# Optimization experiments

Measured on AMD Instinct MI355X. Metric: run time of the kernel, lower is better.

## Reference

```python
import jax, jax.numpy as jnp
import numpy as np

HIDDEN = 1024
N_HEADS = 16
HEAD_DIM = HIDDEN // N_HEADS


def _rope_tables(seq_len, dim, dtype):
    inv_freq = 1.0 / (10000.0 ** (jnp.arange(0, dim, 2, dtype=jnp.float32) / dim))
    t = jnp.arange(seq_len, dtype=jnp.float32)
    freqs = jnp.einsum('i,j->ij', t, inv_freq)          # [S, dim/2]
    emb = jnp.concatenate([freqs, freqs], axis=-1)       # [S, dim]
    cos = jnp.cos(emb)[None, :, None, :].astype(dtype)   # [1, S, 1, dim]
    sin = jnp.sin(emb)[None, :, None, :].astype(dtype)
    return cos, sin


def _rotate_half(x):
    x1, x2 = x[..., : x.shape[-1] // 2], x[..., x.shape[-1] // 2 :]
    return jnp.concatenate([-x2, x1], axis=-1)


def setup_inputs() -> dict:
    key = jax.random.key(0)
    ks = jax.random.split(key, 9)
    s = 1.0 / np.sqrt(HIDDEN)
    return {
        'x': jax.random.normal(ks[0], (2, 2048, HIDDEN), dtype=jnp.float32),
        'q_w': jax.random.uniform(ks[1], (HIDDEN, HIDDEN), jnp.float32, -s, s),
        'q_b': jax.random.uniform(ks[2], (HIDDEN,), jnp.float32, -s, s),
        'k_w': jax.random.uniform(ks[3], (HIDDEN, HIDDEN), jnp.float32, -s, s),
        'k_b': jax.random.uniform(ks[4], (HIDDEN,), jnp.float32, -s, s),
        'v_w': jax.random.uniform(ks[5], (HIDDEN, HIDDEN), jnp.float32, -s, s),
        'v_b': jax.random.uniform(ks[6], (HIDDEN,), jnp.float32, -s, s),
        'o_w': jax.random.uniform(ks[7], (HIDDEN, HIDDEN), jnp.float32, -s, s),
        'o_b': jax.random.uniform(ks[8], (HIDDEN,), jnp.float32, -s, s),
    }


def reference(x, q_w, q_b, k_w, k_b, v_w, v_b, o_w, o_b):
    B, S, _ = x.shape
    scale = HEAD_DIM ** -0.5
    # projections (torch Linear: x @ W.T + b)
    q = (x @ q_w.T + q_b).reshape(B, S, N_HEADS, HEAD_DIM)
    k = (x @ k_w.T + k_b).reshape(B, S, N_HEADS, HEAD_DIM)
    v = (x @ v_w.T + v_b).reshape(B, S, N_HEADS, HEAD_DIM)
    # RoPE
    cos, sin = _rope_tables(S, HEAD_DIM, x.dtype)
    q = q * cos + _rotate_half(q) * sin
    k = k * cos + _rotate_half(k) * sin
    # attention: [B, H, S, S]
    scores = jnp.einsum('bqhd,bkhd->bhqk', q, k) * scale
    attn = jax.nn.softmax(scores, axis=-1)
    out = jnp.einsum('bhqk,bkhd->bqhd', attn, v).reshape(B, S, HIDDEN)
    return out @ o_w.T + o_b
```

## Files before the change

kernel.cpp:

```cpp
#include <hip/hip_runtime.h>
#include <hip/hip_bf16.h>


#define SEQ    2048
#define BATCH  2
#define NHEADS 16
#define HDIM   64
#define HID    1024
#define NTOK   (BATCH*SEQ)

typedef __bf16 bf16x8 __attribute__((ext_vector_type(8)));
typedef float  f32x4  __attribute__((ext_vector_type(4)));
typedef unsigned short u16x8 __attribute__((ext_vector_type(8)));

__device__ __forceinline__ unsigned short bfc(float x) {
  return __builtin_bit_cast(unsigned short, (__bf16)x);
}
#define EXP2(x) __builtin_amdgcn_exp2f(x)

__device__ __forceinline__ void gload16(const void* gptr, void* ldsptr) {
  typedef __attribute__((address_space(3))) unsigned int as3_uint;
  typedef const __attribute__((address_space(1))) unsigned int as1_uint;
  __builtin_amdgcn_global_load_lds(
      (as1_uint*)(unsigned long long)gptr,
      (as3_uint*)(unsigned int)(unsigned long long)ldsptr,
      16, 0, 0);
}

__device__ __forceinline__ void cvt8(const float* __restrict__ s,
                                     unsigned short* __restrict__ d, int i) {
  float4 a = *reinterpret_cast<const float4*>(s + i);
  float4 b = *reinterpret_cast<const float4*>(s + i + 4);
  u16x8 o;
  o[0] = bfc(a.x); o[1] = bfc(a.y); o[2] = bfc(a.z); o[3] = bfc(a.w);
  o[4] = bfc(b.x); o[5] = bfc(b.y); o[6] = bfc(b.z); o[7] = bfc(b.w);
  *reinterpret_cast<u16x8*>(d + i) = o;
}

__global__ __launch_bounds__(256) void prep(
    const float* __restrict__ x,
    const float* __restrict__ qw, const float* __restrict__ kw,
    const float* __restrict__ vw, const float* __restrict__ ow,
    unsigned short* __restrict__ xb,
    unsigned short* __restrict__ wqb, unsigned short* __restrict__ wkb,
    unsigned short* __restrict__ wvb, unsigned short* __restrict__ wob,
    float* __restrict__ ct, float* __restrict__ st)
{
  const int XN = NTOK * HID / 8;
  const int WN = HID * HID / 8;
  int tid = blockIdx.x * 256 + threadIdx.x;
  if (tid < XN) {
    cvt8(x, xb, tid * 8);
  } else if (tid < XN + 4 * WN) {
    int r = tid - XN;
    int which = r >> 17;
    int i = (r & (WN - 1)) * 8;
    const float* s = (which == 0) ? qw : (which == 1) ? kw : (which == 2) ? vw : ow;
    unsigned short* d = (which == 0) ? wqb : (which == 1) ? wkb : (which == 2) ? wvb : wob;
    cvt8(s, d, i);
  } else {
    int idx = tid - (XN + 4 * WN);
    if (idx < SEQ * 32) {
      int p = idx >> 5, j = idx & 31;
      float inv = powf(10000.0f, -(float)(2 * j) * (1.0f / 64.0f));
      float a = (float)p * inv;
      ct[idx] = cosf(a);
      st[idx] = sinf(a);
    }
  }
}

__global__ __launch_bounds__(256) void gemm_qkv(
    const unsigned short* __restrict__ X,
    const unsigned short* __restrict__ Wq, const unsigned short* __restrict__ Wk,
    const unsigned short* __restrict__ Wv,
    const float* __restrict__ bq, const float* __restrict__ bk, const float* __restrict__ bv,
    const float* __restrict__ ct, const float* __restrict__ st,
    unsigned short* __restrict__ Qo, unsigned short* __restrict__ Ko,
    unsigned short* __restrict__ VTo)
{
  __shared__ unsigned short LSH[16384];
  const int z = blockIdx.z;
  const unsigned short* W = (z == 0) ? Wq : (z == 1) ? Wk : Wv;
  const float* bias = (z == 0) ? bq : (z == 1) ? bk : bv;
  const int tm = blockIdx.x, tn = blockIdx.y;
  const int t = threadIdx.x, w = t >> 6, l = t & 63;
  const int wm = w >> 1, wn = w & 1, g = l >> 4;

  f32x4 acc[4][4] = {};

  const int arow0 = tm * 128, brow0 = tn * 128;
  const int s0 = w * 2, s1 = w * 2 + 1;
  const int r0 = s0 * 16 + (l >> 2), r1 = s1 * 16 + (l >> 2);
  const int kc = (l & 3) * 8;

#define GSTAGE(buf, k0)                                                            \
  {                                                                                \
    gload16(X + (long)(arow0 + r0) * HID + (k0) + kc, LSH + (buf) * 4096 + s0 * 512); \
    gload16(X + (long)(arow0 + r1) * HID + (k0) + kc, LSH + (buf) * 4096 + s1 * 512); \
    gload16(W + (long)(brow0 + r0) * HID + (k0) + kc, LSH + 8192 + (buf) * 4096 + s0 * 512); \
    gload16(W + (long)(brow0 + r1) * HID + (k0) + kc, LSH + 8192 + (buf) * 4096 + s1 * 512); \
  }

  GSTAGE(0, 0)
  asm volatile("s_waitcnt vmcnt(0)" ::: "memory");
  __builtin_amdgcn_s_barrier();
  int cur = 0;
  for (int k0 = 0; k0 < HID; k0 += 32) {
    if (k0 + 32 < HID) GSTAGE(cur ^ 1, k0 + 32)
    bf16x8 af[4], bfr[4];
#pragma unroll
    for (int fm = 0; fm < 4; ++fm)
      af[fm] = *reinterpret_cast<const bf16x8*>(
          LSH + cur * 4096 + (wm * 64 + fm * 16 + (l & 15)) * 32 + g * 8);
#pragma unroll
    for (int fn = 0; fn < 4; ++fn)
      bfr[fn] = *reinterpret_cast<const bf16x8*>(
          LSH + 8192 + cur * 4096 + (wn * 64 + fn * 16 + (l & 15)) * 32 + g * 8);
    __builtin_amdgcn_s_setprio(1);
#pragma unroll
    for (int fm = 0; fm < 4; ++fm)
#pragma unroll
      for (int fn = 0; fn < 4; ++fn)
        acc[fm][fn] = __builtin_amdgcn_mfma_f32_16x16x32_bf16(af[fm], bfr[fn], acc[fm][fn], 0, 0, 0);
    __builtin_amdgcn_s_setprio(0);
    asm volatile("s_waitcnt vmcnt(0)" ::: "memory");
    __builtin_amdgcn_s_barrier();
    cur ^= 1;
  }
#undef GSTAGE

  const int colb = brow0 + wn * 64;
  float bsv[4];
#pragma unroll
  for (int fn = 0; fn < 4; ++fn) bsv[fn] = bias[colb + fn * 16 + (l & 15)];

  if (z == 2) {
#pragma unroll
    for (int fm = 0; fm < 4; ++fm) {
      int tok = wm * 64 + fm * 16 + g * 4;
#pragma unroll
      for (int fn = 0; fn < 4; ++fn) {
        int col = wn * 64 + fn * 16 + (l & 15);
        unsigned int u0 = (unsigned int)bfc(acc[fm][fn][0] + bsv[fn]) |
                          ((unsigned int)bfc(acc[fm][fn][1] + bsv[fn]) << 16);
        unsigned int u1 = (unsigned int)bfc(acc[fm][fn][2] + bsv[fn]) |
                          ((unsigned int)bfc(acc[fm][fn][3] + bsv[fn]) << 16);
        uint2 uv; uv.x = u0; uv.y = u1;
        *reinterpret_cast<uint2*>(&LSH[col * 128 + (tok ^ ((col & 7) << 3))]) = uv;
      }
    }
    __syncthreads();
    const int bb = arow0 >> 11, stok = arow0 & (SEQ - 1);
#pragma unroll
    for (int p8 = 0; p8 < 8; ++p8) {
      int col = p8 * 16 + (t >> 4);
      int soff = (t & 15) * 8;
      uint4 v = *reinterpret_cast<const uint4*>(&LSH[col * 128 + (soff ^ ((col & 7) << 3))]);
      int hh = (brow0 + col) >> 6;
      int dd = col & 63;
      unsigned short* dst = VTo + ((long)(bb * NHEADS + hh) * HDIM + dd) * SEQ + stok + soff;
      *reinterpret_cast<uint4*>(dst) = v;
    }
    return;
  }

  unsigned short* Out = (z == 0) ? Qo : Ko;
  const int h = colb >> 6;
#pragma unroll
  for (int fm = 0; fm < 4; ++fm) {
#pragma unroll
    for (int r = 0; r < 4; ++r) {
      int grow = arow0 + wm * 64 + fm * 16 + g * 4 + r;
      int b = grow >> 11, sidx = grow & (SEQ - 1);
      unsigned short* ob = Out + ((long)(b * NHEADS + h) * SEQ + sidx) * HDIM;
#pragma unroll
      for (int fn2 = 0; fn2 < 2; ++fn2) {
        int d1 = fn2 * 16 + (l & 15);
        float v1 = acc[fm][fn2][r] + bsv[fn2];
        float v2 = acc[fm][fn2 + 2][r] + bsv[fn2 + 2];
        float c = ct[sidx * 32 + d1], sn = st[sidx * 32 + d1];
        float o1 = v1 * c - v2 * sn;
        float o2 = v2 * c + v1 * sn;
        if (z == 0) { o1 *= 0.18033688f; o2 *= 0.18033688f; }
        ob[d1] = bfc(o1);
        ob[d1 + 32] = bfc(o2);
      }
    }
  }
}

__global__ __launch_bounds__(256) void attn(
    const unsigned short* __restrict__ Qb,
    const unsigned short* __restrict__ Kb,
    const unsigned short* __restrict__ VTb,
    unsigned short* __restrict__ Ob)
{
  __shared__ unsigned short Kl[2][64 * 64];
  __shared__ unsigned short Vl[2][64 * 64];
  __shared__ unsigned short Pl[4][32 * 64];
  const int bh = blockIdx.x, qt = blockIdx.y;
  const int b = bh >> 4, h = bh & 15;
  const int t = threadIdx.x, w = t >> 6, l = t & 63;
  const long hb = (long)bh * SEQ * HDIM;
  const int g = l >> 4;
  const int swz = (l & 7) << 4;

  const int q0 = qt * 128 + w * 32;
  bf16x8 qf[2][2];
#pragma unroll
  for (int f = 0; f < 2; ++f)
#pragma unroll
    for (int ks = 0; ks < 2; ++ks)
      qf[f][ks] = *reinterpret_cast<const bf16x8*>(
          Qb + hb + (long)(q0 + f * 16 + (l & 15)) * HDIM + ks * 32 + g * 8);

  f32x4 oacc[2][4] = {};
  float lrun[2] = {0.f, 0.f};

  const int srow = l >> 3;
  const int scol = (((l & 7) * 16) ^ ((l >> 3) << 4)) >> 1;
#define STAGE(buf, kt)                                                          \
  {                                                                             \
    gload16(Kb + hb + (long)((kt) + w * 16 + srow) * HDIM + scol,               \
            (char*)Kl[buf] + w * 2048);                                         \
    gload16(Kb + hb + (long)((kt) + w * 16 + 8 + srow) * HDIM + scol,           \
            (char*)Kl[buf] + w * 2048 + 1024);                                  \
    gload16(VTb + hb + (long)(w * 16 + srow) * SEQ + (kt) + scol,               \
            (char*)Vl[buf] + w * 2048);                                         \
    gload16(VTb + hb + (long)(w * 16 + 8 + srow) * SEQ + (kt) + scol,           \
            (char*)Vl[buf] + w * 2048 + 1024);                                  \
  }

  STAGE(0, 0)
  asm volatile("s_waitcnt vmcnt(0)" ::: "memory");
  __builtin_amdgcn_s_barrier();
  int cur = 0;

  for (int it = 0; it < SEQ / 64; ++it) {
    if (it + 1 < SEQ / 64) STAGE(cur ^ 1, (it + 1) * 64)

    f32x4 sa[2][4];
#pragma unroll
    for (int f = 0; f < 2; ++f)
#pragma unroll
      for (int fn = 0; fn < 4; ++fn) sa[f][fn] = f32x4{0.f, 0.f, 0.f, 0.f};
    __builtin_amdgcn_s_setprio(1);
#pragma unroll
    for (int fnK = 0; fnK < 4; ++fnK) {
#pragma unroll
      for (int ks = 0; ks < 2; ++ks) {
        bf16x8 kf = *reinterpret_cast<const bf16x8*>(
            (char*)Kl[cur] + (fnK * 16 + (l & 15)) * 128 + ((ks * 64 + g * 16) ^ swz));
        sa[0][fnK] = __builtin_amdgcn_mfma_f32_16x16x32_bf16(kf, qf[0][ks], sa[0][fnK], 0, 0, 0);
        sa[1][fnK] = __builtin_amdgcn_mfma_f32_16x16x32_bf16(kf, qf[1][ks], sa[1][fnK], 0, 0, 0);
      }
    }
    __builtin_amdgcn_s_setprio(0);

#pragma unroll
    for (int f = 0; f < 2; ++f) {
      float rs = 0.f;
#pragma unroll
      for (int fn = 0; fn < 4; ++fn)
#pragma unroll
        for (int r = 0; r < 4; ++r) {
          float p = EXP2(sa[f][fn][r]);
          sa[f][fn][r] = p;
          rs += p;
        }
      lrun[f] += rs;
    }

#pragma unroll
    for (int f = 0; f < 2; ++f) {
      char* pw = (char*)Pl[w] + (f * 16 + (l & 15)) * 128;
#pragma unroll
      for (int fn = 0; fn < 4; ++fn) {
        unsigned int u0 = (unsigned int)bfc(sa[f][fn][0]) | ((unsigned int)bfc(sa[f][fn][1]) << 16);
        unsigned int u1 = (unsigned int)bfc(sa[f][fn][2]) | ((unsigned int)bfc(sa[f][fn][3]) << 16);
        uint2 uv; uv.x = u0; uv.y = u1;
        *reinterpret_cast<uint2*>(pw + ((fn * 32 + g * 8) ^ swz)) = uv;
      }
    }

    bf16x8 pf[2][2];
#pragma unroll
    for (int f = 0; f < 2; ++f)
#pragma unroll
      for (int ks = 0; ks < 2; ++ks)
        pf[f][ks] = *reinterpret_cast<const bf16x8*>(
            (char*)Pl[w] + (f * 16 + (l & 15)) * 128 + ((ks * 64 + g * 16) ^ swz));
    __builtin_amdgcn_s_setprio(1);
#pragma unroll
    for (int fnD = 0; fnD < 4; ++fnD) {
#pragma unroll
      for (int ks = 0; ks < 2; ++ks) {
        bf16x8 vf = *reinterpret_cast<const bf16x8*>(
            (char*)Vl[cur] + (fnD * 16 + (l & 15)) * 128 + ((ks * 64 + g * 16) ^ swz));
        oacc[0][fnD] = __builtin_amdgcn_mfma_f32_16x16x32_bf16(vf, pf[0][ks], oacc[0][fnD], 0, 0, 0);
        oacc[1][fnD] = __builtin_amdgcn_mfma_f32_16x16x32_bf16(vf, pf[1][ks], oacc[1][fnD], 0, 0, 0);
      }
    }
    __builtin_amdgcn_s_setprio(0);

    asm volatile("s_waitcnt vmcnt(0)" ::: "memory");
    __builtin_amdgcn_s_barrier();
    cur ^= 1;
  }
#undef STAGE

#pragma unroll
  for (int f = 0; f < 2; ++f) {
    float lr = lrun[f];
    lr += __shfl_xor(lr, 16);
    lr += __shfl_xor(lr, 32);
    float inv = 1.0f / lr;
    int q = q0 + f * 16 + (l & 15);
    unsigned short* op = Ob + (long)(b * SEQ + q) * HID + h * HDIM;
#pragma unroll
    for (int fnD = 0; fnD < 4; ++fnD) {
      unsigned int lo = (unsigned int)bfc(oacc[f][fnD][0] * inv) |
                        ((unsigned int)bfc(oacc[f][fnD][1] * inv) << 16);
      unsigned int hi = (unsigned int)bfc(oacc[f][fnD][2] * inv) |
                        ((unsigned int)bfc(oacc[f][fnD][3] * inv) << 16);
      uint2 uv; uv.x = lo; uv.y = hi;
      *reinterpret_cast<uint2*>(op + fnD * 16 + g * 4) = uv;
    }
  }
}

__global__ __launch_bounds__(256) void gemm_o(
    const unsigned short* __restrict__ A,
    const unsigned short* __restrict__ W,
    const float* __restrict__ bias,
    float* __restrict__ Out)
{
  __shared__ unsigned short Al[2][128 * 32];
  __shared__ unsigned short Bl[2][128 * 32];
  const int tm = blockIdx.x, tn = blockIdx.y;
  const int t = threadIdx.x, w = t >> 6, l = t & 63;
  const int wm = w >> 1, wn = w & 1;

  f32x4 acc[4][4] = {};
  const int arow0 = tm * 128, brow0 = tn * 128;
  const int s0 = w * 2, s1 = w * 2 + 1;
  const int r0 = s0 * 16 + (l >> 2), r1 = s1 * 16 + (l >> 2);
  const int kc = (l & 3) * 8;

#define GSTAGE(buf, k0)                                                       \
  {                                                                           \
    gload16(A + (long)(arow0 + r0) * HID + (k0) + kc, Al[buf] + s0 * 512);    \
    gload16(A + (long)(arow0 + r1) * HID + (k0) + kc, Al[buf] + s1 * 512);    \
    gload16(W + (long)(brow0 + r0) * HID + (k0) + kc, Bl[buf] + s0 * 512);    \
    gload16(W + (long)(brow0 + r1) * HID + (k0) + kc, Bl[buf] + s1 * 512);    \
  }

  GSTAGE(0, 0)
  asm volatile("s_waitcnt vmcnt(0)" ::: "memory");
  __builtin_amdgcn_s_barrier();
  int cur = 0;
  for (int k0 = 0; k0 < HID; k0 += 32) {
    if (k0 + 32 < HID) GSTAGE(cur ^ 1, k0 + 32)
    bf16x8 af[4], bfr[4];
#pragma unroll
    for (int fm = 0; fm < 4; ++fm)
      af[fm] = *reinterpret_cast<const bf16x8*>(Al[cur] + (wm * 64 + fm * 16 + (l & 15)) * 32 + (l >> 4) * 8);
#pragma unroll
    for (int fn = 0; fn < 4; ++fn)
      bfr[fn] = *reinterpret_cast<const bf16x8*>(Bl[cur] + (wn * 64 + fn * 16 + (l & 15)) * 32 + (l >> 4) * 8);
    __builtin_amdgcn_s_setprio(1);
#pragma unroll
    for (int fm = 0; fm < 4; ++fm)
#pragma unroll
      for (int fn = 0; fn < 4; ++fn)
        acc[fm][fn] = __builtin_amdgcn_mfma_f32_16x16x32_bf16(af[fm], bfr[fn], acc[fm][fn], 0, 0, 0);
    __builtin_amdgcn_s_setprio(0);
    asm volatile("s_waitcnt vmcnt(0)" ::: "memory");
    __builtin_amdgcn_s_barrier();
    cur ^= 1;
  }
#undef GSTAGE

  const int colb = brow0 + wn * 64;
  float bsv[4];
#pragma unroll
  for (int fn = 0; fn < 4; ++fn) bsv[fn] = bias[colb + fn * 16 + (l & 15)];
#pragma unroll
  for (int fm = 0; fm < 4; ++fm)
#pragma unroll
    for (int r = 0; r < 4; ++r) {
      int grow = arow0 + wm * 64 + fm * 16 + (l >> 4) * 4 + r;
#pragma unroll
      for (int fn = 0; fn < 4; ++fn)
        Out[(long)grow * HID + colb + fn * 16 + (l & 15)] = acc[fm][fn][r] + bsv[fn];
    }
}

extern "C" void kernel_launch(void* const* d_in, const int* in_sizes, int n_in,
                              void* d_out, int out_size, void* d_ws, size_t ws_size,
                              hipStream_t stream) {
  const float* x  = (const float*)d_in[0];
  const float* qw = (const float*)d_in[1];
  const float* qb = (const float*)d_in[2];
  const float* kw = (const float*)d_in[3];
  const float* kb = (const float*)d_in[4];
  const float* vw = (const float*)d_in[5];
  const float* vb = (const float*)d_in[6];
  const float* ow = (const float*)d_in[7];
  const float* ob = (const float*)d_in[8];
  float* out = (float*)d_out;

  char* p = (char*)d_ws;
  unsigned short* xb  = (unsigned short*)p; p += (size_t)NTOK * HID * 2;
  unsigned short* wqb = (unsigned short*)p; p += (size_t)HID * HID * 2;
  unsigned short* wkb = (unsigned short*)p; p += (size_t)HID * HID * 2;
  unsigned short* wvb = (unsigned short*)p; p += (size_t)HID * HID * 2;
  unsigned short* wob = (unsigned short*)p; p += (size_t)HID * HID * 2;
  unsigned short* Qb  = (unsigned short*)p; p += (size_t)NTOK * HID * 2;
  unsigned short* Kb  = (unsigned short*)p; p += (size_t)NTOK * HID * 2;
  unsigned short* VTb = (unsigned short*)p; p += (size_t)NTOK * HID * 2;
  float* ct = (float*)p; p += (size_t)SEQ * 32 * 4;
  float* st = (float*)p; p += (size_t)SEQ * 32 * 4;
  unsigned short* Ab  = xb;

  const int XN = NTOK * HID / 8, WN = HID * HID / 8;
  const int prep_threads = XN + 4 * WN + SEQ * 32;
  prep<<<dim3((prep_threads + 255) / 256), 256, 0, stream>>>(
      x, qw, kw, vw, ow, xb, wqb, wkb, wvb, wob, ct, st);

  gemm_qkv<<<dim3(NTOK / 128, HID / 128, 3), 256, 0, stream>>>(
      xb, wqb, wkb, wvb, qb, kb, vb, ct, st, Qb, Kb, VTb);

  attn<<<dim3(BATCH * NHEADS, SEQ / 128), 256, 0, stream>>>(Qb, Kb, VTb, Ab);

  gemm_o<<<dim3(NTOK / 128, HID / 128), 256, 0, stream>>>(Ab, wob, ob, out);
}
```

Measured before the change: 124.8 us.

## Software-pipeline attention QK and PV across iterations; shrink output GEMM N tile

The attention loop is restructured so that the QK^T MFMAs for tile i run in the same phase as the PV MFMAs for tile i-1. V gets a triple buffer so the staged V tile stays live for one extra iteration, and pointer increments replace recomputed addresses. This is meant to hide the softmax/P round-trip latency behind independent matrix work. Separately, the output GEMM N tile drops from 128 to 64, doubling the block count for better CU occupancy at the cost of more A-tile reloads.

```diff
diff --git a/kernel.cpp b/kernel.cpp
--- a/kernel.cpp
+++ b/kernel.cpp
@@ -197,7 +197,7 @@
     unsigned short* __restrict__ Ob)
 {
   __shared__ unsigned short Kl[2][64 * 64];
-  __shared__ unsigned short Vl[2][64 * 64];
+  __shared__ unsigned short Vl[3][64 * 64];
   __shared__ unsigned short Pl[4][32 * 64];
   const int bh = blockIdx.x, qt = blockIdx.y;
   const int b = bh >> 4, h = bh & 15;
@@ -218,97 +218,126 @@
   f32x4 oacc[2][4] = {};
   float lrun[2] = {0.f, 0.f};
 
+  const int rowq = (l & 15) * 128;
+  const int colx0 = (g * 16) ^ swz;
+  const int colx1 = (64 + g * 16) ^ swz;
+  char* const Pw = (char*)Pl + w * 4096;
+
   const int srow = l >> 3;
   const int scol = (((l & 7) * 16) ^ ((l >> 3) << 4)) >> 1;
-#define STAGE(buf, kt)                                                          \
-  {                                                                             \
-    gload16(Kb + hb + (long)((kt) + w * 16 + srow) * HDIM + scol,               \
-            (char*)Kl[buf] + w * 2048);                                         \
-    gload16(Kb + hb + (long)((kt) + w * 16 + 8 + srow) * HDIM + scol,           \
-            (char*)Kl[buf] + w * 2048 + 1024);                                  \
-    gload16(VTb + hb + (long)(w * 16 + srow) * SEQ + (kt) + scol,               \
-            (char*)Vl[buf] + w * 2048);                                         \
-    gload16(VTb + hb + (long)(w * 16 + 8 + srow) * SEQ + (kt) + scol,           \
-            (char*)Vl[buf] + w * 2048 + 1024);                                  \
-  }
+  const unsigned short* kp0 = Kb + hb + (long)(w * 16 + srow) * HDIM + scol;
+  const unsigned short* kp1 = kp0 + 8 * HDIM;
+  const unsigned short* vp0 = VTb + hb + (long)(w * 16 + srow) * SEQ + scol;
+  const unsigned short* vp1 = vp0 + 8 * SEQ;
+
+#define STAGE(kbuf, vbuf)                                              \
+  {                                                                    \
+    gload16(kp0, (char*)Kl + (kbuf) * 8192 + w * 2048);                \
+    gload16(kp1, (char*)Kl + (kbuf) * 8192 + w * 2048 + 1024);         \
+    gload16(vp0, (char*)Vl + (vbuf) * 8192 + w * 2048);                \
+    gload16(vp1, (char*)Vl + (vbuf) * 8192 + w * 2048 + 1024);         \
+    kp0 += 64 * HDIM; kp1 += 64 * HDIM; vp0 += 64; vp1 += 64;          \
+  }
+
+#define QK(kbuf)                                                                  \
+  _Pragma("unroll")                                                               \
+  for (int f = 0; f < 2; ++f)                                                     \
+    _Pragma("unroll")                                                             \
+    for (int fn = 0; fn < 4; ++fn) sa[f][fn] = f32x4{0.f, 0.f, 0.f, 0.f};         \
+  _Pragma("unroll")                                                               \
+  for (int fnK = 0; fnK < 4; ++fnK) {                                             \
+    const char* kb_ = (char*)Kl + (kbuf) * 8192 + fnK * 2048 + rowq;              \
+    bf16x8 kf0 = *reinterpret_cast<const bf16x8*>(kb_ + colx0);                   \
+    bf16x8 kf1 = *reinterpret_cast<const bf16x8*>(kb_ + colx1);                   \
+    sa[0][fnK] = __builtin_amdgcn_mfma_f32_16x16x32_bf16(kf0, qf[0][0], sa[0][fnK], 0, 0, 0); \
+    sa[0][fnK] = __builtin_amdgcn_mfma_f32_16x16x32_bf16(kf1, qf[0][1], sa[0][fnK], 0, 0, 0); \
+    sa[1][fnK] = __builtin_amdgcn_mfma_f32_16x16x32_bf16(kf0, qf[1][0], sa[1][fnK], 0, 0, 0); \
+    sa[1][fnK] = __builtin_amdgcn_mfma_f32_16x16x32_bf16(kf1, qf[1][1], sa[1][fnK], 0, 0, 0); \
+  }
+
+#define PFREAD                                                                    \
+  _Pragma("unroll")                                                               \
+  for (int f = 0; f < 2; ++f) {                                                   \
+    pf[f][0] = *reinterpret_cast<const bf16x8*>(Pw + f * 2048 + rowq + colx0);    \
+    pf[f][1] = *reinterpret_cast<const bf16x8*>(Pw + f * 2048 + rowq + colx1);    \
+  }
+
+#define PVSTEP(vbuf)                                                              \
+  _Pragma("unroll")                                                               \
+  for (int fnD = 0; fnD < 4; ++fnD) {                                             \
+    const char* vb_ = (char*)Vl + (vbuf) * 8192 + fnD * 2048 + rowq;              \
+    bf16x8 vf0 = *reinterpret_cast<const bf16x8*>(vb_ + colx0);                   \
+    bf16x8 vf1 = *reinterpret_cast<const bf16x8*>(vb_ + colx1);                   \
+    oacc[0][fnD] = __builtin_amdgcn_mfma_f32_16x16x32_bf16(vf0, pf[0][0], oacc[0][fnD], 0, 0, 0); \
+    oacc[0][fnD] = __builtin_amdgcn_mfma_f32_16x16x32_bf16(vf1, pf[0][1], oacc[0][fnD], 0, 0, 0); \
+    oacc[1][fnD] = __builtin_amdgcn_mfma_f32_16x16x32_bf16(vf0, pf[1][0], oacc[1][fnD], 0, 0, 0); \
+    oacc[1][fnD] = __builtin_amdgcn_mfma_f32_16x16x32_bf16(vf1, pf[1][1], oacc[1][fnD], 0, 0, 0); \
+  }
+
+#define SOFTPACK                                                                  \
+  _Pragma("unroll")                                                               \
+  for (int f = 0; f < 2; ++f) {                                                   \
+    float rs = 0.f;                                                               \
+    _Pragma("unroll")                                                             \
+    for (int fn = 0; fn < 4; ++fn)                                                \
+      _Pragma("unroll")                                                           \
+      for (int r = 0; r < 4; ++r) {                                               \
+        float p = EXP2(sa[f][fn][r]);                                             \
+        sa[f][fn][r] = p;                                                         \
+        rs += p;                                                                  \
+      }                                                                           \
+    lrun[f] += rs;                                                                \
+    char* pw_ = Pw + f * 2048 + rowq;                                             \
+    _Pragma("unroll")                                                             \
+    for (int fn = 0; fn < 4; ++fn) {                                              \
+      unsigned int u0 = (unsigned int)bfc(sa[f][fn][0]) | ((unsigned int)bfc(sa[f][fn][1]) << 16); \
+      unsigned int u1 = (unsigned int)bfc(sa[f][fn][2]) | ((unsigned int)bfc(sa[f][fn][3]) << 16); \
+      uint2 uv; uv.x = u0; uv.y = u1;                                             \
+      *reinterpret_cast<uint2*>(pw_ + ((fn * 32 + g * 8) ^ swz)) = uv;            \
+    }                                                                             \
+  }
+
+  f32x4 sa[2][4];
+  bf16x8 pf[2][2];
 
   STAGE(0, 0)
   asm volatile("s_waitcnt vmcnt(0)" ::: "memory");
   __builtin_amdgcn_s_barrier();
-  int cur = 0;
-
-  for (int it = 0; it < SEQ / 64; ++it) {
-    if (it + 1 < SEQ / 64) STAGE(cur ^ 1, (it + 1) * 64)
-
-    f32x4 sa[2][4];
-#pragma unroll
-    for (int f = 0; f < 2; ++f)
-#pragma unroll
-      for (int fn = 0; fn < 4; ++fn) sa[f][fn] = f32x4{0.f, 0.f, 0.f, 0.f};
+
+  STAGE(1, 1)
+  __builtin_amdgcn_s_setprio(1);
+  QK(0)
+  __builtin_amdgcn_s_setprio(0);
+  SOFTPACK
+  asm volatile("s_waitcnt vmcnt(0)" ::: "memory");
+  __builtin_amdgcn_s_barrier();
+
+  int kcur = 1, vr = 0, vw = 2;
+  for (int it = 1; it < SEQ / 64; ++it) {
+    PFREAD
+    if (it + 1 < SEQ / 64) STAGE(kcur ^ 1, vw)
     __builtin_amdgcn_s_setprio(1);
-#pragma unroll
-    for (int fnK = 0; fnK < 4; ++fnK) {
-#pragma unroll
-      for (int ks = 0; ks < 2; ++ks) {
-        bf16x8 kf = *reinterpret_cast<const bf16x8*>(
-            (char*)Kl[cur] + (fnK * 16 + (l & 15)) * 128 + ((ks * 64 + g * 16) ^ swz));
-        sa[0][fnK] = __builtin_amdgcn_mfma_f32_16x16x32_bf16(kf, qf[0][ks], sa[0][fnK], 0, 0, 0);
-        sa[1][fnK] = __builtin_amdgcn_mfma_f32_16x16x32_bf16(kf, qf[1][ks], sa[1][fnK], 0, 0, 0);
-      }
-    }
+    QK(kcur)
+    PVSTEP(vr)
     __builtin_amdgcn_s_setprio(0);
-
-#pragma unroll
-    for (int f = 0; f < 2; ++f) {
-      float rs = 0.f;
-#pragma unroll
-      for (int fn = 0; fn < 4; ++fn)
-#pragma unroll
-        for (int r = 0; r < 4; ++r) {
-          float p = EXP2(sa[f][fn][r]);
-          sa[f][fn][r] = p;
-          rs += p;
-        }
-      lrun[f] += rs;
-    }
-
-#pragma unroll
-    for (int f = 0; f < 2; ++f) {
-      char* pw = (char*)Pl[w] + (f * 16 + (l & 15)) * 128;
-#pragma unroll
-      for (int fn = 0; fn < 4; ++fn) {
-        unsigned int u0 = (unsigned int)bfc(sa[f][fn][0]) | ((unsigned int)bfc(sa[f][fn][1]) << 16);
-        unsigned int u1 = (unsigned int)bfc(sa[f][fn][2]) | ((unsigned int)bfc(sa[f][fn][3]) << 16);
-        uint2 uv; uv.x = u0; uv.y = u1;
-        *reinterpret_cast<uint2*>(pw + ((fn * 32 + g * 8) ^ swz)) = uv;
-      }
-    }
-
-    bf16x8 pf[2][2];
-#pragma unroll
-    for (int f = 0; f < 2; ++f)
-#pragma unroll
-      for (int ks = 0; ks < 2; ++ks)
-        pf[f][ks] = *reinterpret_cast<const bf16x8*>(
-            (char*)Pl[w] + (f * 16 + (l & 15)) * 128 + ((ks * 64 + g * 16) ^ swz));
-    __builtin_amdgcn_s_setprio(1);
-#pragma unroll
-    for (int fnD = 0; fnD < 4; ++fnD) {
-#pragma unroll
-      for (int ks = 0; ks < 2; ++ks) {
-        bf16x8 vf = *reinterpret_cast<const bf16x8*>(
-            (char*)Vl[cur] + (fnD * 16 + (l & 15)) * 128 + ((ks * 64 + g * 16) ^ swz));
-        oacc[0][fnD] = __builtin_amdgcn_mfma_f32_16x16x32_bf16(vf, pf[0][ks], oacc[0][fnD], 0, 0, 0);
-        oacc[1][fnD] = __builtin_amdgcn_mfma_f32_16x16x32_bf16(vf, pf[1][ks], oacc[1][fnD], 0, 0, 0);
-      }
-    }
-    __builtin_amdgcn_s_setprio(0);
-
+    SOFTPACK
     asm volatile("s_waitcnt vmcnt(0)" ::: "memory");
     __builtin_amdgcn_s_barrier();
-    cur ^= 1;
-  }
+    kcur ^= 1;
+    vr = (vr == 2) ? 0 : vr + 1;
+    vw = (vw == 2) ? 0 : vw + 1;
+  }
+
+  PFREAD
+  __builtin_amdgcn_s_setprio(1);
+  PVSTEP(vr)
+  __builtin_amdgcn_s_setprio(0);
+
 #undef STAGE
+#undef QK
+#undef PFREAD
+#undef PVSTEP
+#undef SOFTPACK
 
 #pragma unroll
   for (int f = 0; f < 2; ++f) {
@@ -337,23 +366,23 @@
     float* __restrict__ Out)
 {
   __shared__ unsigned short Al[2][128 * 32];
-  __shared__ unsigned short Bl[2][128 * 32];
+  __shared__ unsigned short Bl[2][64 * 32];
   const int tm = blockIdx.x, tn = blockIdx.y;
   const int t = threadIdx.x, w = t >> 6, l = t & 63;
   const int wm = w >> 1, wn = w & 1;
 
-  f32x4 acc[4][4] = {};
-  const int arow0 = tm * 128, brow0 = tn * 128;
+  f32x4 acc[4][2] = {};
+  const int arow0 = tm * 128, brow0 = tn * 64;
   const int s0 = w * 2, s1 = w * 2 + 1;
   const int r0 = s0 * 16 + (l >> 2), r1 = s1 * 16 + (l >> 2);
+  const int rb = w * 16 + (l >> 2);
   const int kc = (l & 3) * 8;
 
 #define GSTAGE(buf, k0)                                                       \
   {                                                                           \
     gload16(A + (long)(arow0 + r0) * HID + (k0) + kc, Al[buf] + s0 * 512);    \
     gload16(A + (long)(arow0 + r1) * HID + (k0) + kc, Al[buf] + s1 * 512);    \
-    gload16(W + (long)(brow0 + r0) * HID + (k0) + kc, Bl[buf] + s0 * 512);    \
-    gload16(W + (long)(brow0 + r1) * HID + (k0) + kc, Bl[buf] + s1 * 512);    \
+    gload16(W + (long)(brow0 + rb) * HID + (k0) + kc, Bl[buf] + w * 512);     \
   }
 
   GSTAGE(0, 0)
@@ -362,18 +391,18 @@
   int cur = 0;
   for (int k0 = 0; k0 < HID; k0 += 32) {
     if (k0 + 32 < HID) GSTAGE(cur ^ 1, k0 + 32)
-    bf16x8 af[4], bfr[4];
+    bf16x8 af[4], bfr[2];
 #pragma unroll
     for (int fm = 0; fm < 4; ++fm)
       af[fm] = *reinterpret_cast<const bf16x8*>(Al[cur] + (wm * 64 + fm * 16 + (l & 15)) * 32 + (l >> 4) * 8);
 #pragma unroll
-    for (int fn = 0; fn < 4; ++fn)
-      bfr[fn] = *reinterpret_cast<const bf16x8*>(Bl[cur] + (wn * 64 + fn * 16 + (l & 15)) * 32 + (l >> 4) * 8);
+    for (int fn = 0; fn < 2; ++fn)
+      bfr[fn] = *reinterpret_cast<const bf16x8*>(Bl[cur] + (wn * 32 + fn * 16 + (l & 15)) * 32 + (l >> 4) * 8);
     __builtin_amdgcn_s_setprio(1);
 #pragma unroll
     for (int fm = 0; fm < 4; ++fm)
 #pragma unroll
-      for (int fn = 0; fn < 4; ++fn)
+      for (int fn = 0; fn < 2; ++fn)
         acc[fm][fn] = __builtin_amdgcn_mfma_f32_16x16x32_bf16(af[fm], bfr[fn], acc[fm][fn], 0, 0, 0);
     __builtin_amdgcn_s_setprio(0);
     asm volatile("s_waitcnt vmcnt(0)" ::: "memory");
@@ -382,17 +411,17 @@
   }
 #undef GSTAGE
 
-  const int colb = brow0 + wn * 64;
-  float bsv[4];
-#pragma unroll
-  for (int fn = 0; fn < 4; ++fn) bsv[fn] = bias[colb + fn * 16 + (l & 15)];
+  const int colb = brow0 + wn * 32;
+  float bsv[2];
+#pragma unroll
+  for (int fn = 0; fn < 2; ++fn) bsv[fn] = bias[colb + fn * 16 + (l & 15)];
 #pragma unroll
   for (int fm = 0; fm < 4; ++fm)
 #pragma unroll
     for (int r = 0; r < 4; ++r) {
       int grow = arow0 + wm * 64 + fm * 16 + (l >> 4) * 4 + r;
 #pragma unroll
-      for (int fn = 0; fn < 4; ++fn)
+      for (int fn = 0; fn < 2; ++fn)
         Out[(long)grow * HID + colb + fn * 16 + (l & 15)] = acc[fm][fn][r] + bsv[fn];
     }
 }
@@ -434,5 +463,5 @@
 
   attn<<<dim3(BATCH * NHEADS, SEQ / 128), 256, 0, stream>>>(Qb, Kb, VTb, Ab);
 
-  gemm_o<<<dim3(NTOK / 128, HID / 128), 256, 0, stream>>>(Ab, wob, ob, out);
-}
+  gemm_o<<<dim3(NTOK / 128, HID / 64), 256, 0, stream>>>(Ab, wob, ob, out);
+}
```

New measurement: 119.8 us. 4.0% less time.
